# Optimization experiments

Measured on AMD Instinct MI355X. Metric: run time of the kernel, lower is better.

## Reference

```python
import jax, jax.numpy as jnp
import numpy as np

BATCH, IN_F, OUT_F = 1024, 512, 512
GRID_SIZE, SPLINE_ORDER = 32, 3
P_DEACTIVATE = 0.1


def b_splines(x, grid, k):
    """x: (n, in), grid: (in, G+2k+1) -> bases (n, in, G+k). Cox-de Boor recursion."""
    x = x[..., None]  # (n, in, 1)
    bases = ((x >= grid[:, :-1]) & (x < grid[:, 1:])).astype(x.dtype)
    for j in range(1, k + 1):
        left = (x - grid[:, : -(j + 1)]) / (grid[:, j:-1] - grid[:, : -(j + 1)])
        right = (grid[:, j + 1:] - x) / (grid[:, j + 1:] - grid[:, 1:-j])
        bases = left * bases[..., :-1] + right * bases[..., 1:]
    return bases


def setup_inputs() -> dict:
    key = jax.random.key(0)
    k1, k2, k3, k4, k5 = jax.random.split(key, 5)
    # uniform extended grid over [-1, 1], same for every input feature
    h = 2.0 / GRID_SIZE
    knots = np.arange(-SPLINE_ORDER, GRID_SIZE + SPLINE_ORDER + 1, dtype=np.float32) * h - 1.0
    grid = jnp.asarray(np.tile(knots, (IN_F, 1)))  # (in, G+2k+1)
    return {
        "x": jax.random.normal(k1, (BATCH, IN_F), jnp.float32),
        "base_weight": jax.random.normal(k2, (OUT_F, IN_F), jnp.float32) * 0.05,
        "spline_weight": jax.random.normal(k3, (OUT_F, IN_F, GRID_SIZE + SPLINE_ORDER), jnp.float32) * 0.1,
        "spline_scaler": jax.random.normal(k4, (OUT_F, IN_F), jnp.float32),
        "grid": grid,
        "deactivate_mask": jax.random.bernoulli(k5, P_DEACTIVATE, (OUT_F, IN_F)),
    }


def reference(x, base_weight, spline_weight, spline_scaler, grid, deactivate_mask):
    k = SPLINE_ORDER
    weights = spline_weight * spline_scaler[..., None]  # scaled_spline_weight (o, i, c)
    # base path: F.linear(silu(x), base_weight)
    base_out = jax.nn.silu(x) @ base_weight.T  # (b, o)
    # spline path
    bases = b_splines(x, grid, k)  # (b, i, c)
    contrib = jnp.einsum('bic,oic->boi', bases, weights)  # (b, o, i)
    # linear fallback from spline values at grid endpoints
    gmin = grid[:, k].min()
    gmax = grid[:, -k - 1].max()
    ends_x = jnp.stack([gmin, gmax])[:, None] * jnp.ones((1, x.shape[1]), x.dtype)  # (2, i)
    y_ends = jnp.einsum('nic,oic->noi', b_splines(ends_x, grid, k), weights)  # (2, o, i)
    y_start, y_end = y_ends[0], y_ends[1]
    dx = gmax - gmin
    degenerate = jnp.abs(dx) < 1e-8
    a = jnp.where(degenerate, 0.0, (y_end - y_start) / jnp.where(degenerate, 1.0, dx))  # (o, i)
    b = y_start - a * gmin
    lin = a[None] * x[:, None, :] + b[None]  # (b, o, i)
    final = jnp.where(deactivate_mask[None], lin, contrib)
    return base_out + final.sum(axis=2)
```

## Files before the change

### kernel.cpp

```cpp
#include <hip/hip_runtime.h>
#include <hip/hip_bf16.h>


typedef unsigned short u16;
typedef unsigned int u32;
typedef unsigned long long u64;
typedef __attribute__((ext_vector_type(8))) short short8;
typedef __attribute__((ext_vector_type(4))) float floatx4;

#define IN_F 512
#define OUT_F 512
#define BATCH 1024
#define K_SPLINE (IN_F * 36)
#define K_BASE_OFF K_SPLINE
#define K_LIN_OFF (K_SPLINE + IN_F)
#define K_TOT (K_SPLINE + 2 * IN_F)
#define SPLITS 32
#define MN (BATCH * OUT_F)

static __device__ inline u16 f2b(float f) {
  union { float f; u32 u; } v; v.f = f;
  u32 r = v.u + 0x7FFFu + ((v.u >> 16) & 1u);
  return (u16)(r >> 16);
}
static __device__ inline float b2f(u32 lo16) {
  union { u32 u; float f; } v; v.u = lo16 << 16; return v.f;
}

__global__ __launch_bounds__(256) void prep_kernel(
    const float* __restrict__ bw, const float* __restrict__ sw,
    const float* __restrict__ sc, const void* __restrict__ maskp,
    const float* __restrict__ x, u16* __restrict__ B,
    float* __restrict__ bias_part, u16* __restrict__ A) {
  __shared__ __align__(16) u64 lds64[1120 * 4];
  __shared__ int sflag;
  __shared__ float ws4[4];
  int blk = blockIdx.x, t = threadIdx.x;

  if (blk >= 1024) {
    int bix = blk - 1024;
    int b = bix >> 1;
    int i0 = (bix & 1) << 8;
    int i = i0 + t;
    float xv = x[(size_t)b * IN_F + i];

    u64* myrow = lds64 + t * 9;
#pragma unroll
    for (int j = 0; j < 9; ++j) myrow[j] = 0;

    int mc = (int)floorf((xv + 1.1875f) * 16.0f);
    float gm = (float)mc * 0.0625f - 1.1875f;
    if (xv < gm) { mc -= 1; gm -= 0.0625f; }
    else if (xv >= gm + 0.0625f) { mc += 1; gm += 0.0625f; }
    if (mc >= 0 && mc <= 37) {
      float t_ = (xv - gm) * 16.0f;
      float t2 = t_ * t_, t3 = t2 * t_;
      float omt = 1.0f - t_;
      u16 r0 = f2b(omt * omt * omt * (1.0f / 6.0f));
      u16 r1 = f2b((3.0f * t3 - 6.0f * t2 + 4.0f) * (1.0f / 6.0f));
      u16 r2 = f2b((-3.0f * t3 + 3.0f * t2 + 3.0f * t_ + 1.0f) * (1.0f / 6.0f));
      float f0 = b2f(r0), f1 = b2f(r1), f2 = b2f(r2);
      u16 bv[4] = {r0, r1, r2, f2b(1.0f - f0 - f1 - f2)};
      u16* lds_u = (u16*)lds64;
#pragma unroll
      for (int j = 0; j < 4; ++j) {
        int c = mc - 3 + j;
        if ((u32)c < 35u) lds_u[t * 36 + c] = bv[j];
      }
    }
    __syncthreads();

    u64* dstA = (u64*)(A + (size_t)b * K_TOT + (size_t)i0 * 36);
#pragma unroll
    for (int j = 0; j < 9; ++j) dstA[j * 256 + t] = lds64[j * 256 + t];

    float sl = xv / (1.0f + __expf(-xv));
    A[(size_t)b * K_TOT + K_BASE_OFF + i] = f2b(sl);
    A[(size_t)b * K_TOT + K_LIN_OFF + i] = f2b(xv);
    return;
  }

  float* lds_f = (float*)lds64;
  u16* lds_u = (u16*)lds64;
  int id = blk * 256 + t;
  int o = id >> 9, i = id & 511;
  int i0 = (blk & 1) * 256;

  const float* swb = sw + ((size_t)o * 512 + i0) * 35;
  const floatx4* sw4 = (const floatx4*)swb;
  floatx4* lds4 = (floatx4*)lds_f;
#pragma unroll
  for (int j = 0; j < 8; ++j) lds4[j * 256 + t] = sw4[j * 256 + t];
  if (t < 192) lds4[8 * 256 + t] = sw4[8 * 256 + t];

  const u32* mw = (const u32*)maskp;
  if (t == 0) sflag = 0;
  __syncthreads();
  if (t < 64) {
    u32 w2 = mw[blk * 64 + t];
    if ((w2 & 0xFFFFFF00u) && w2 != 0x3F800000u) atomicOr(&sflag, 1);
  }
  __syncthreads();
  int fl = sflag;
  if (!(fl & 1)) {
    u32 w1 = mw[blk * 256 + t];
    if (w1 == 0x3F800000u) atomicOr(&sflag, 2);
  }
  __syncthreads();
  fl = sflag;
  bool mk;
  if (fl & 1)      mk = ((const unsigned char*)maskp)[id] != 0;
  else if (fl & 2) mk = ((const float*)maskp)[id] != 0.0f;
  else             mk = ((const int*)maskp)[id] != 0;

  float s = sc[id];
  float w[35];
#pragma unroll
  for (int c = 0; c < 35; ++c) w[c] = lds_f[t * 35 + c] * s;
  __syncthreads();

  float ys = (w[0] + 4.0f * w[1] + w[2]) * (1.0f / 6.0f);
  float ye = (w[32] + 4.0f * w[33] + w[34]) * (1.0f / 6.0f);
  float a = (ye - ys) * 0.5f;
  float bl = ys + a;

#pragma unroll
  for (int c = 0; c < 35; ++c) lds_u[t * 36 + c] = f2b(mk ? 0.0f : w[c]);
  lds_u[t * 36 + 35] = 0;

  B[(size_t)o * K_TOT + K_BASE_OFF + i] = f2b(bw[id]);
  B[(size_t)o * K_TOT + K_LIN_OFF + i] = f2b(mk ? a : 0.0f);

  float v = mk ? bl : 0.0f;
#pragma unroll
  for (int off = 32; off >= 1; off >>= 1) v += __shfl_down(v, off);
  if ((t & 63) == 0) ws4[t >> 6] = v;
  __syncthreads();
  if (t == 0) bias_part[blk] = ws4[0] + ws4[1] + ws4[2] + ws4[3];

  u64* dst = (u64*)(B + (size_t)o * K_TOT + (size_t)i0 * 36);
#pragma unroll
  for (int j = 0; j < 9; ++j) dst[j * 256 + t] = lds64[j * 256 + t];
}

__global__ __launch_bounds__(256, 4) void gemm_fused(const u16* __restrict__ A,
                                                     const u16* __restrict__ Bp,
                                                     u16* __restrict__ P) {
  __shared__ u16 As[128 * 64];
  __shared__ u16 Bs[128 * 64];

  int t = threadIdx.x;
  int id = blockIdx.x;
  int ks = id >> 5, tile = id & 31;
  int bm = tile >> 2, bn = tile & 3;
  int w = t >> 6, l = t & 63;
  int wm = w & 1, wn = w >> 1;

  floatx4 acc[4][4];
#pragma unroll
  for (int p = 0; p < 4; ++p)
#pragma unroll
    for (int q = 0; q < 4; ++q) acc[p][q] = (floatx4)0.0f;

  int nit = (ks < 16) ? 10 : 9;
  int k0s = (ks < 16) ? ks * 640 : 10240 + (ks - 16) * 576;

  int ra = t >> 3;
  int cg = (t & 7) ^ (ra & 7);
  const u16* Agp = A + (size_t)(bm * 128 + ra) * K_TOT + k0s + cg * 8;
  const u16* Bgp = Bp + (size_t)(bn * 128 + ra) * K_TOT + k0s + cg * 8;
  u16* Asp = As + t * 8;
  u16* Bsp = Bs + t * 8;

  int mr = l & 15;
  int cq = l >> 4;

  for (int kk = 0; kk < nit; ++kk) {
#pragma unroll
    for (int p = 0; p < 4; ++p)
      __builtin_amdgcn_global_load_lds(
          (const __attribute__((address_space(1))) void*)(Agp + (size_t)p * 32 * K_TOT),
          (__attribute__((address_space(3))) void*)(Asp + p * 2048), 16, 0, 0);
#pragma unroll
    for (int p = 0; p < 4; ++p)
      __builtin_amdgcn_global_load_lds(
          (const __attribute__((address_space(1))) void*)(Bgp + (size_t)p * 32 * K_TOT),
          (__attribute__((address_space(3))) void*)(Bsp + p * 2048), 16, 0, 0);
    Agp += 64;
    Bgp += 64;
    __syncthreads();

#pragma unroll
    for (int h = 0; h < 2; ++h) {
      short8 af[4], bf[4];
      int c = h * 4 + cq;
#pragma unroll
      for (int tm = 0; tm < 4; ++tm) {
        int row = wm * 64 + tm * 16 + mr;
        af[tm] = *(const short8*)&As[row * 64 + ((c ^ (row & 7)) << 3)];
      }
#pragma unroll
      for (int tn = 0; tn < 4; ++tn) {
        int row = wn * 64 + tn * 16 + mr;
        bf[tn] = *(const short8*)&Bs[row * 64 + ((c ^ (row & 7)) << 3)];
      }
#pragma unroll
      for (int tm = 0; tm < 4; ++tm)
#pragma unroll
        for (int tn = 0; tn < 4; ++tn)
          acc[tm][tn] = __builtin_amdgcn_mfma_f32_16x16x32_bf16(af[tm], bf[tn], acc[tm][tn], 0, 0, 0);
    }
    __syncthreads();
  }

  u16* Pb = P + ((size_t)tile * SPLITS + ks) * 16384;
#pragma unroll
  for (int q = 0; q < 8; ++q) {
    int tm = q >> 1, tn0 = (q & 1) * 2;
    u16 r[8];
#pragma unroll
    for (int z = 0; z < 4; ++z) r[z] = f2b(acc[tm][tn0][z]);
#pragma unroll
    for (int z = 0; z < 4; ++z) r[4 + z] = f2b(acc[tm][tn0 + 1][z]);
    *(short8*)(Pb + q * 2048 + t * 8) = *(short8*)r;
  }
}

__global__ __launch_bounds__(256) void reduce_kernel(const u16* __restrict__ P,
                                                     const float* __restrict__ bias_part,
                                                     float* __restrict__ out) {
  int rid = blockIdx.x * 256 + threadIdx.x;
  int tile = rid >> 11;
  int rem = rid & 2047;
  int q = rem >> 8, t = rem & 255;
  const u16* base = P + (size_t)tile * SPLITS * 16384 + q * 2048 + t * 8;

  float s[8] = {0, 0, 0, 0, 0, 0, 0, 0};
#pragma unroll
  for (int ks = 0; ks < SPLITS; ++ks) {
    short8 v = *(const short8*)(base + (size_t)ks * 16384);
#pragma unroll
    for (int j = 0; j < 8; ++j) s[j] += b2f((u32)(u16)v[j]);
  }

  int w = t >> 6, l = t & 63;
  int wm = w & 1, wn = w >> 1;
  int bm = tile >> 2, bn = tile & 3;
  int row0 = bm * 128 + wm * 64 + ((l >> 4) << 2);
  int col0 = bn * 128 + wn * 64 + (l & 15);
  int tm = q >> 1, tn0 = (q & 1) * 2;
#pragma unroll
  for (int j = 0; j < 8; ++j) {
    int tn = tn0 + (j >> 2), rr = j & 3;
    int row = row0 + tm * 16 + rr;
    int col = col0 + tn * 16;
    float bsv = bias_part[2 * col] + bias_part[2 * col + 1];
    out[(size_t)row * OUT_F + col] = s[j] + bsv;
  }
}

extern "C" void kernel_launch(void* const* d_in, const int* in_sizes, int n_in,
                              void* d_out, int out_size, void* d_ws, size_t ws_size,
                              hipStream_t stream) {
  const float* x  = (const float*)d_in[0];
  const float* bw = (const float*)d_in[1];
  const float* sw = (const float*)d_in[2];
  const float* sc = (const float*)d_in[3];
  const void* mask = d_in[5];

  const size_t B_BYTES = (size_t)OUT_F * K_TOT * 2;
  const size_t BIAS_OFF = B_BYTES;
  const size_t A_OFF = B_BYTES + 8192;
  const size_t A_BYTES = (size_t)BATCH * K_TOT * 2;
  const size_t P_OFF = A_OFF + A_BYTES;

  char* wsb = (char*)d_ws;
  u16* Bpack = (u16*)wsb;
  float* bias_part = (float*)(wsb + BIAS_OFF);
  u16* Adense = (u16*)(wsb + A_OFF);
  u16* P = (u16*)(wsb + P_OFF);

  prep_kernel<<<3072, 256, 0, stream>>>(bw, sw, sc, mask, x, Bpack, bias_part, Adense);
  gemm_fused<<<1024, 256, 0, stream>>>(Adense, Bpack, P);
  reduce_kernel<<<256, 256, 0, stream>>>(P, bias_part, (float*)d_out);
}
```

Baseline: 139.9 us.

## Split prep into separate A/B kernels, pack B rows in registers, remap GEMM tiles

The fused prep kernel is split into an A-side kernel (small LDS, launch bound 8) and a B-side kernel, so the A blocks no longer reserve the large shared-memory footprint of the weight path and can run at higher occupancy. The B-side now builds each bf16 row in registers and writes it to LDS as 64-bit words instead of 16-bit scalar stores. The GEMM block index mapping is also remapped so that consecutive blocks share A/B tiles across split-K slices, which may improve L2 locality. The cost is one extra kernel launch and less overlap between the A and B prep work.

```diff
diff --git a/kernel.cpp b/kernel.cpp
--- a/kernel.cpp
+++ b/kernel.cpp
@@ -27,61 +27,60 @@
   union { u32 u; float f; } v; v.u = lo16 << 16; return v.f;
 }
 
-__global__ __launch_bounds__(256) void prep_kernel(
+__global__ __launch_bounds__(256, 8) void prep_a_kernel(
+    const float* __restrict__ x, u16* __restrict__ A) {
+  __shared__ __align__(16) u64 lds64[256 * 9];
+  int bix = blockIdx.x, t = threadIdx.x;
+  int b = bix >> 1;
+  int i0 = (bix & 1) << 8;
+  int i = i0 + t;
+  float xv = x[(size_t)b * IN_F + i];
+
+  u64* myrow = lds64 + t * 9;
+#pragma unroll
+  for (int j = 0; j < 9; ++j) myrow[j] = 0;
+
+  int mc = (int)floorf((xv + 1.1875f) * 16.0f);
+  float gm = (float)mc * 0.0625f - 1.1875f;
+  if (xv < gm) { mc -= 1; gm -= 0.0625f; }
+  else if (xv >= gm + 0.0625f) { mc += 1; gm += 0.0625f; }
+  if (mc >= 0 && mc <= 37) {
+    float t_ = (xv - gm) * 16.0f;
+    float t2 = t_ * t_, t3 = t2 * t_;
+    float omt = 1.0f - t_;
+    u16 r0 = f2b(omt * omt * omt * (1.0f / 6.0f));
+    u16 r1 = f2b((3.0f * t3 - 6.0f * t2 + 4.0f) * (1.0f / 6.0f));
+    u16 r2 = f2b((-3.0f * t3 + 3.0f * t2 + 3.0f * t_ + 1.0f) * (1.0f / 6.0f));
+    float f0 = b2f(r0), f1 = b2f(r1), f2 = b2f(r2);
+    u16 bv[4] = {r0, r1, r2, f2b(1.0f - f0 - f1 - f2)};
+    u16* lds_u = (u16*)lds64;
+#pragma unroll
+    for (int j = 0; j < 4; ++j) {
+      int c = mc - 3 + j;
+      if ((u32)c < 35u) lds_u[t * 36 + c] = bv[j];
+    }
+  }
+  __syncthreads();
+
+  u64* dstA = (u64*)(A + (size_t)b * K_TOT + (size_t)i0 * 36);
+#pragma unroll
+  for (int j = 0; j < 9; ++j) dstA[j * 256 + t] = lds64[j * 256 + t];
+
+  float sl = xv / (1.0f + __expf(-xv));
+  A[(size_t)b * K_TOT + K_BASE_OFF + i] = f2b(sl);
+  A[(size_t)b * K_TOT + K_LIN_OFF + i] = f2b(xv);
+}
+
+__global__ __launch_bounds__(256) void prep_b_kernel(
     const float* __restrict__ bw, const float* __restrict__ sw,
     const float* __restrict__ sc, const void* __restrict__ maskp,
-    const float* __restrict__ x, u16* __restrict__ B,
-    float* __restrict__ bias_part, u16* __restrict__ A) {
+    u16* __restrict__ B, float* __restrict__ bias_part) {
   __shared__ __align__(16) u64 lds64[1120 * 4];
   __shared__ int sflag;
   __shared__ float ws4[4];
   int blk = blockIdx.x, t = threadIdx.x;
 
-  if (blk >= 1024) {
-    int bix = blk - 1024;
-    int b = bix >> 1;
-    int i0 = (bix & 1) << 8;
-    int i = i0 + t;
-    float xv = x[(size_t)b * IN_F + i];
-
-    u64* myrow = lds64 + t * 9;
-#pragma unroll
-    for (int j = 0; j < 9; ++j) myrow[j] = 0;
-
-    int mc = (int)floorf((xv + 1.1875f) * 16.0f);
-    float gm = (float)mc * 0.0625f - 1.1875f;
-    if (xv < gm) { mc -= 1; gm -= 0.0625f; }
-    else if (xv >= gm + 0.0625f) { mc += 1; gm += 0.0625f; }
-    if (mc >= 0 && mc <= 37) {
-      float t_ = (xv - gm) * 16.0f;
-      float t2 = t_ * t_, t3 = t2 * t_;
-      float omt = 1.0f - t_;
-      u16 r0 = f2b(omt * omt * omt * (1.0f / 6.0f));
-      u16 r1 = f2b((3.0f * t3 - 6.0f * t2 + 4.0f) * (1.0f / 6.0f));
-      u16 r2 = f2b((-3.0f * t3 + 3.0f * t2 + 3.0f * t_ + 1.0f) * (1.0f / 6.0f));
-      float f0 = b2f(r0), f1 = b2f(r1), f2 = b2f(r2);
-      u16 bv[4] = {r0, r1, r2, f2b(1.0f - f0 - f1 - f2)};
-      u16* lds_u = (u16*)lds64;
-#pragma unroll
-      for (int j = 0; j < 4; ++j) {
-        int c = mc - 3 + j;
-        if ((u32)c < 35u) lds_u[t * 36 + c] = bv[j];
-      }
-    }
-    __syncthreads();
-
-    u64* dstA = (u64*)(A + (size_t)b * K_TOT + (size_t)i0 * 36);
-#pragma unroll
-    for (int j = 0; j < 9; ++j) dstA[j * 256 + t] = lds64[j * 256 + t];
-
-    float sl = xv / (1.0f + __expf(-xv));
-    A[(size_t)b * K_TOT + K_BASE_OFF + i] = f2b(sl);
-    A[(size_t)b * K_TOT + K_LIN_OFF + i] = f2b(xv);
-    return;
-  }
-
   float* lds_f = (float*)lds64;
-  u16* lds_u = (u16*)lds64;
   int id = blk * 256 + t;
   int o = id >> 9, i = id & 511;
   int i0 = (blk & 1) * 256;
@@ -124,9 +123,13 @@
   float a = (ye - ys) * 0.5f;
   float bl = ys + a;
 
-#pragma unroll
-  for (int c = 0; c < 35; ++c) lds_u[t * 36 + c] = f2b(mk ? 0.0f : w[c]);
-  lds_u[t * 36 + 35] = 0;
+  union { u16 r16[36]; u64 r64[9]; } ur;
+#pragma unroll
+  for (int c = 0; c < 35; ++c) ur.r16[c] = f2b(mk ? 0.0f : w[c]);
+  ur.r16[35] = 0;
+  u64* myrow = lds64 + t * 9;
+#pragma unroll
+  for (int j = 0; j < 9; ++j) myrow[j] = ur.r64[j];
 
   B[(size_t)o * K_TOT + K_BASE_OFF + i] = f2b(bw[id]);
   B[(size_t)o * K_TOT + K_LIN_OFF + i] = f2b(mk ? a : 0.0f);
@@ -150,17 +153,21 @@
   __shared__ u16 Bs[128 * 64];
 
   int t = threadIdx.x;
-  int id = blockIdx.x;
-  int ks = id >> 5, tile = id & 31;
-  int bm = tile >> 2, bn = tile & 3;
+  int p = blockIdx.x;
+  int x_ = p & 7, j = p >> 3;
+  int bm = j & 7, idx = j >> 3;
+  int bn = x_ & 3;
+  int ks = 2 * idx + (x_ >> 2);
+  int tile = (bm << 2) | bn;
+
   int w = t >> 6, l = t & 63;
   int wm = w & 1, wn = w >> 1;
 
   floatx4 acc[4][4];
 #pragma unroll
-  for (int p = 0; p < 4; ++p)
-#pragma unroll
-    for (int q = 0; q < 4; ++q) acc[p][q] = (floatx4)0.0f;
+  for (int pp = 0; pp < 4; ++pp)
+#pragma unroll
+    for (int q = 0; q < 4; ++q) acc[pp][q] = (floatx4)0.0f;
 
   int nit = (ks < 16) ? 10 : 9;
   int k0s = (ks < 16) ? ks * 640 : 10240 + (ks - 16) * 576;
@@ -177,15 +184,15 @@
 
   for (int kk = 0; kk < nit; ++kk) {
 #pragma unroll
-    for (int p = 0; p < 4; ++p)
+    for (int q = 0; q < 4; ++q)
       __builtin_amdgcn_global_load_lds(
-          (const __attribute__((address_space(1))) void*)(Agp + (size_t)p * 32 * K_TOT),
-          (__attribute__((address_space(3))) void*)(Asp + p * 2048), 16, 0, 0);
-#pragma unroll
-    for (int p = 0; p < 4; ++p)
+          (const __attribute__((address_space(1))) void*)(Agp + (size_t)q * 32 * K_TOT),
+          (__attribute__((address_space(3))) void*)(Asp + q * 2048), 16, 0, 0);
+#pragma unroll
+    for (int q = 0; q < 4; ++q)
       __builtin_amdgcn_global_load_lds(
-          (const __attribute__((address_space(1))) void*)(Bgp + (size_t)p * 32 * K_TOT),
-          (__attribute__((address_space(3))) void*)(Bsp + p * 2048), 16, 0, 0);
+          (const __attribute__((address_space(1))) void*)(Bgp + (size_t)q * 32 * K_TOT),
+          (__attribute__((address_space(3))) void*)(Bsp + q * 2048), 16, 0, 0);
     Agp += 64;
     Bgp += 64;
     __syncthreads();
@@ -280,7 +287,8 @@
   u16* Adense = (u16*)(wsb + A_OFF);
   u16* P = (u16*)(wsb + P_OFF);
 
-  prep_kernel<<<3072, 256, 0, stream>>>(bw, sw, sc, mask, x, Bpack, bias_part, Adense);
+  prep_a_kernel<<<2048, 256, 0, stream>>>(x, Adense);
+  prep_b_kernel<<<1024, 256, 0, stream>>>(bw, sw, sc, mask, Bpack, bias_part);
   gemm_fused<<<1024, 256, 0, stream>>>(Adense, Bpack, P);
   reduce_kernel<<<256, 256, 0, stream>>>(P, bias_part, (float*)d_out);
 }
```

After: 137.3 us. Within noise of the previous version (-1.8%).

## Double-buffer GEMM LDS stages with even K splits and reordered block mapping

Applied to the files above, without the earlier changes.

The split-K GEMM now uses two 32-wide LDS buffers, so the next K slice is fetched with global_load_lds while MFMAs run on the current one. This replaces the earlier single 64-wide buffer that loaded and then computed with no overlap. K is split evenly as 32×608, the block index is remapped so that consecutive blocks vary the M tile first to share the B tile, and s_setprio is raised around the MFMA burst. The prep kernel also packs each bf16 row in registers and writes it to LDS as 64-bit stores instead of 16-bit ones. The trade-off is twice as many barrier-separated iterations, each with less MFMA work to hide load latency behind.

```diff
diff --git a/kernel.cpp b/kernel.cpp
--- a/kernel.cpp
+++ b/kernel.cpp
@@ -16,6 +16,8 @@
 #define K_LIN_OFF (K_SPLINE + IN_F)
 #define K_TOT (K_SPLINE + 2 * IN_F)
 #define SPLITS 32
+#define KPS 608
+#define NIT 19
 #define MN (BATCH * OUT_F)
 
 static __device__ inline u16 f2b(float f) {
@@ -81,7 +83,6 @@
   }
 
   float* lds_f = (float*)lds64;
-  u16* lds_u = (u16*)lds64;
   int id = blk * 256 + t;
   int o = id >> 9, i = id & 511;
   int i0 = (blk & 1) * 256;
@@ -124,9 +125,13 @@
   float a = (ye - ys) * 0.5f;
   float bl = ys + a;
 
-#pragma unroll
-  for (int c = 0; c < 35; ++c) lds_u[t * 36 + c] = f2b(mk ? 0.0f : w[c]);
-  lds_u[t * 36 + 35] = 0;
+  union { u16 r16[36]; u64 r64[9]; } ur;
+#pragma unroll
+  for (int c = 0; c < 35; ++c) ur.r16[c] = f2b(mk ? 0.0f : w[c]);
+  ur.r16[35] = 0;
+  u64* myrow = lds64 + t * 9;
+#pragma unroll
+  for (int j = 0; j < 9; ++j) myrow[j] = ur.r64[j];
 
   B[(size_t)o * K_TOT + K_BASE_OFF + i] = f2b(bw[id]);
   B[(size_t)o * K_TOT + K_LIN_OFF + i] = f2b(mk ? a : 0.0f);
@@ -146,72 +151,83 @@
 __global__ __launch_bounds__(256, 4) void gemm_fused(const u16* __restrict__ A,
                                                      const u16* __restrict__ Bp,
                                                      u16* __restrict__ P) {
-  __shared__ u16 As[128 * 64];
-  __shared__ u16 Bs[128 * 64];
+  __shared__ u16 As[2][128 * 32];
+  __shared__ u16 Bs[2][128 * 32];
 
   int t = threadIdx.x;
-  int id = blockIdx.x;
-  int ks = id >> 5, tile = id & 31;
-  int bm = tile >> 2, bn = tile & 3;
+  int p = blockIdx.x;
+  int bm = p & 7;
+  int j = p >> 3;
+  int bn = j & 3;
+  int ks = j >> 2;
+  int tile = (bm << 2) | bn;
+
   int w = t >> 6, l = t & 63;
   int wm = w & 1, wn = w >> 1;
 
   floatx4 acc[4][4];
 #pragma unroll
-  for (int p = 0; p < 4; ++p)
-#pragma unroll
-    for (int q = 0; q < 4; ++q) acc[p][q] = (floatx4)0.0f;
-
-  int nit = (ks < 16) ? 10 : 9;
-  int k0s = (ks < 16) ? ks * 640 : 10240 + (ks - 16) * 576;
-
-  int ra = t >> 3;
-  int cg = (t & 7) ^ (ra & 7);
+  for (int pp = 0; pp < 4; ++pp)
+#pragma unroll
+    for (int q = 0; q < 4; ++q) acc[pp][q] = (floatx4)0.0f;
+
+  int k0s = ks * KPS;
+
+  int ra = t >> 2;
+  int cg = (t & 3) ^ (ra & 3);
   const u16* Agp = A + (size_t)(bm * 128 + ra) * K_TOT + k0s + cg * 8;
   const u16* Bgp = Bp + (size_t)(bn * 128 + ra) * K_TOT + k0s + cg * 8;
-  u16* Asp = As + t * 8;
-  u16* Bsp = Bs + t * 8;
 
   int mr = l & 15;
   int cq = l >> 4;
 
-  for (int kk = 0; kk < nit; ++kk) {
-#pragma unroll
-    for (int p = 0; p < 4; ++p)
-      __builtin_amdgcn_global_load_lds(
-          (const __attribute__((address_space(1))) void*)(Agp + (size_t)p * 32 * K_TOT),
-          (__attribute__((address_space(3))) void*)(Asp + p * 2048), 16, 0, 0);
-#pragma unroll
-    for (int p = 0; p < 4; ++p)
-      __builtin_amdgcn_global_load_lds(
-          (const __attribute__((address_space(1))) void*)(Bgp + (size_t)p * 32 * K_TOT),
-          (__attribute__((address_space(3))) void*)(Bsp + p * 2048), 16, 0, 0);
-    Agp += 64;
-    Bgp += 64;
+#define STAGE(buf, kk)                                                          \
+  do {                                                                          \
+    const u16* a_ = Agp + (kk) * 32;                                            \
+    const u16* b_ = Bgp + (kk) * 32;                                            \
+    __builtin_amdgcn_global_load_lds(                                           \
+        (const __attribute__((address_space(1))) void*)a_,                      \
+        (__attribute__((address_space(3))) void*)(&As[buf][t * 8]), 16, 0, 0);  \
+    __builtin_amdgcn_global_load_lds(                                           \
+        (const __attribute__((address_space(1))) void*)(a_ + (size_t)64 * K_TOT),\
+        (__attribute__((address_space(3))) void*)(&As[buf][2048 + t * 8]), 16, 0, 0);\
+    __builtin_amdgcn_global_load_lds(                                           \
+        (const __attribute__((address_space(1))) void*)b_,                      \
+        (__attribute__((address_space(3))) void*)(&Bs[buf][t * 8]), 16, 0, 0);  \
+    __builtin_amdgcn_global_load_lds(                                           \
+        (const __attribute__((address_space(1))) void*)(b_ + (size_t)64 * K_TOT),\
+        (__attribute__((address_space(3))) void*)(&Bs[buf][2048 + t * 8]), 16, 0, 0);\
+  } while (0)
+
+  STAGE(0, 0);
+  __syncthreads();
+
+  for (int kk = 0; kk < NIT; ++kk) {
+    int cur = kk & 1;
+    if (kk + 1 < NIT) STAGE(cur ^ 1, kk + 1);
+
+    short8 af[4], bf[4];
+#pragma unroll
+    for (int tm = 0; tm < 4; ++tm) {
+      int row = wm * 64 + tm * 16 + mr;
+      af[tm] = *(const short8*)&As[cur][row * 32 + ((cq ^ (row & 3)) << 3)];
+    }
+#pragma unroll
+    for (int tn = 0; tn < 4; ++tn) {
+      int row = wn * 64 + tn * 16 + mr;
+      bf[tn] = *(const short8*)&Bs[cur][row * 32 + ((cq ^ (row & 3)) << 3)];
+    }
+    __builtin_amdgcn_s_setprio(1);
+#pragma unroll
+    for (int tm = 0; tm < 4; ++tm)
+#pragma unroll
+      for (int tn = 0; tn < 4; ++tn)
+        acc[tm][tn] = __builtin_amdgcn_mfma_f32_16x16x32_bf16(af[tm], bf[tn], acc[tm][tn], 0, 0, 0);
+    __builtin_amdgcn_s_setprio(0);
+
     __syncthreads();
-
-#pragma unroll
-    for (int h = 0; h < 2; ++h) {
-      short8 af[4], bf[4];
-      int c = h * 4 + cq;
-#pragma unroll
-      for (int tm = 0; tm < 4; ++tm) {
-        int row = wm * 64 + tm * 16 + mr;
-        af[tm] = *(const short8*)&As[row * 64 + ((c ^ (row & 7)) << 3)];
-      }
-#pragma unroll
-      for (int tn = 0; tn < 4; ++tn) {
-        int row = wn * 64 + tn * 16 + mr;
-        bf[tn] = *(const short8*)&Bs[row * 64 + ((c ^ (row & 7)) << 3)];
-      }
-#pragma unroll
-      for (int tm = 0; tm < 4; ++tm)
-#pragma unroll
-        for (int tn = 0; tn < 4; ++tn)
-          acc[tm][tn] = __builtin_amdgcn_mfma_f32_16x16x32_bf16(af[tm], bf[tn], acc[tm][tn], 0, 0, 0);
-    }
-    __syncthreads();
-  }
+  }
+#undef STAGE
 
   u16* Pb = P + ((size_t)tile * SPLITS + ks) * 16384;
 #pragma unroll
```

Measured after the change: 142.2 us. Within noise of the previous version (+1.6%).
